# Optimization experiments

Hardware: AMD Instinct MI355X
Metric: run time of the kernel (lower is better)

Reference implementation:

```python
import jax, jax.numpy as jnp
import numpy as np

B, N, D, H = 2, 2048, 768, 12
HD = D // H  # 64


def apply_rotary_embed(x, thetas):
    # x: (..., N, HD), thetas: (N, HD) broadcast over leading dims
    x1, x2 = jnp.split(x, 2, axis=-1)
    x_rot = jnp.concatenate([-x2, x1], axis=-1)
    return x * jnp.cos(thetas) + x_rot * jnp.sin(thetas)


def setup_inputs() -> dict:
    key = jax.random.key(0)
    ks = jax.random.split(key, 5)
    s = 0.02
    return {
        "x": jax.random.normal(ks[0], (B, N, D), dtype=jnp.float32),
        "pos_embed": jax.random.normal(ks[1], (N, HD), dtype=jnp.float32),
        "Wqkv": jax.random.normal(ks[2], (3 * D, D), dtype=jnp.float32) * s,
        "Wproj": jax.random.normal(ks[3], (D, D), dtype=jnp.float32) * s,
        "bproj": jnp.zeros((D,), dtype=jnp.float32),
    }


def reference(x, pos_embed, Wqkv, Wproj, bproj):
    Bb, Nn, Dd = x.shape
    # fused QKV projection (torch Linear: x @ W.T), no bias
    qkv = jnp.einsum('bnd,ed->bne', x, Wqkv)                 # (B, N, 3D)
    qkv = qkv.reshape(Bb, Nn, 3, H, HD).transpose(2, 0, 3, 1, 4)  # (3, B, H, N, HD)
    q, k, v = qkv[0], qkv[1], qkv[2]
    # rotary embedding on q and k
    q = apply_rotary_embed(q, pos_embed)
    k = apply_rotary_embed(k, pos_embed)
    # scaled dot-product attention (non-causal, no mask, no dropout)
    scale = 1.0 / jnp.sqrt(jnp.asarray(HD, dtype=x.dtype))
    scores = jnp.einsum('bhqd,bhkd->bhqk', q, k) * scale     # (B, H, N, N)
    attn = jax.nn.softmax(scores, axis=-1)
    out = jnp.einsum('bhqk,bhkd->bhqd', attn, v)             # (B, H, N, HD)
    out = out.transpose(0, 2, 1, 3).reshape(Bb, Nn, Dd)      # (B, N, D)
    # output projection (with bias)
    return jnp.einsum('bnd,ed->bne', out, Wproj) + bproj
```

## Files before the change

### kernel.cpp

```cpp
#include <hip/hip_runtime.h>
#include <stdint.h>

typedef __attribute__((ext_vector_type(8))) short short8;
typedef __attribute__((ext_vector_type(4))) float floatx4;
typedef __attribute__((ext_vector_type(16))) float floatx16;

#define BB 2
#define NN 2048
#define DD 768
#define HH 12
#define HDD 64
#define MM (BB*NN)

__device__ __forceinline__ unsigned short f2bf(float f) {
  unsigned int u = __builtin_bit_cast(unsigned int, f);
  u += 0x7fffu + ((u >> 16) & 1u);
  return (unsigned short)(u >> 16);
}
__device__ __forceinline__ float bf2f(unsigned short u) {
  unsigned int v = ((unsigned int)u) << 16;
  return __builtin_bit_cast(float, v);
}

__device__ __forceinline__ void gld16(const unsigned short* g, unsigned short* l) {
  __builtin_amdgcn_global_load_lds(
      (const __attribute__((address_space(1))) void*)g,
      (__attribute__((address_space(3))) void*)l, 16, 0, 0);
}

__global__ void cvt_all(const float* __restrict__ x, const float* __restrict__ wq,
                        const float* __restrict__ wp, unsigned short* __restrict__ xb,
                        unsigned short* __restrict__ wqb, unsigned short* __restrict__ wpb) {
  const int n1 = MM*DD/4, n2 = 3*DD*DD/4, n3 = DD*DD/4;
  int i = blockIdx.x * blockDim.x + threadIdx.x;
  const float* s; unsigned short* d; int j;
  if (i < n1)            { s = x;  d = xb;  j = i; }
  else if (i < n1+n2)    { s = wq; d = wqb; j = i - n1; }
  else if (i < n1+n2+n3) { s = wp; d = wpb; j = i - n1 - n2; }
  else return;
  float4 v = reinterpret_cast<const float4*>(s)[j];
  unsigned int lo = (unsigned int)f2bf(v.x) | ((unsigned int)f2bf(v.y) << 16);
  unsigned int hi = (unsigned int)f2bf(v.z) | ((unsigned int)f2bf(v.w) << 16);
  reinterpret_cast<uint2*>(d)[j] = make_uint2(lo, hi);
}

template<int MODE, int MT>
__global__ __launch_bounds__(256) void gemm_bt(
    const unsigned short* __restrict__ A,
    const unsigned short* __restrict__ Bt,
    void* __restrict__ Cout, const float* __restrict__ bias,
    int Nn, int K,
    const float* __restrict__ pos,
    unsigned short* __restrict__ qb2, unsigned short* __restrict__ kb2,
    unsigned short* __restrict__ vb2)
{
  constexpr int MTC = MT / 32;
  __shared__ __align__(16) unsigned short as_[MT*32];
  __shared__ __align__(16) unsigned short bs_[128*32];
  const int t = threadIdx.x;
  const int w = t >> 6, lane = t & 63;
  const int quad = lane >> 4, l16 = lane & 15;
  const int wm = (w >> 1) * (MT/2), wn = (w & 1) * 64;
  const int m0 = blockIdx.y * MT, n0 = blockIdx.x * 128;

  const floatx4 fz = {0.f, 0.f, 0.f, 0.f};
  floatx4 acc[MTC][4];
#pragma unroll
  for (int mt = 0; mt < MTC; mt++)
#pragma unroll
    for (int nt = 0; nt < 4; nt++) acc[mt][nt] = fz;

  for (int k0 = 0; k0 < K; k0 += 32) {
    __syncthreads();
#pragma unroll
    for (int i = 0; i < MT/64; i++) {
      int c = t + i * 256;
      gld16(&A[(size_t)(m0 + (c >> 2))*K + k0 + (c & 3)*8], &as_[c*8]);
    }
#pragma unroll
    for (int i = 0; i < 2; i++) {
      int c = t + i * 256;
      gld16(&Bt[(size_t)(n0 + (c >> 2))*K + k0 + (c & 3)*8], &bs_[c*8]);
    }
    __syncthreads();
    short8 af[MTC], bfr[4];
#pragma unroll
    for (int mt = 0; mt < MTC; mt++)
      af[mt] = *reinterpret_cast<const short8*>(&as_[(wm + mt*16 + l16)*32 + quad*8]);
#pragma unroll
    for (int nt = 0; nt < 4; nt++)
      bfr[nt] = *reinterpret_cast<const short8*>(&bs_[(wn + nt*16 + l16)*32 + quad*8]);
#pragma unroll
    for (int mt = 0; mt < MTC; mt++)
#pragma unroll
      for (int nt = 0; nt < 4; nt++)
        acc[mt][nt] = __builtin_amdgcn_mfma_f32_16x16x32_bf16(af[mt], bfr[nt], acc[mt][nt], 0, 0, 0);
  }
  if (MODE == 2) {
    const int region = n0 / DD;
    const int nl0 = n0 - region * DD;
    const int head = (nl0 + wn) / HDD;
    if (region < 2) {
#pragma unroll
      for (int mt = 0; mt < MTC; mt++)
#pragma unroll
        for (int r = 0; r < 4; r++) {
          int gm = m0 + wm + mt*16 + quad*4 + r;
          int bq = gm >> 11, nseq = gm & (NN-1);
          size_t base = ((size_t)(bq*HH + head)*NN + nseq) * HDD;
#pragma unroll
          for (int nt = 0; nt < 2; nt++) {
            int hd = nt*16 + l16;
            float t1 = pos[nseq*HDD + hd], t2 = pos[nseq*HDD + hd + 32];
            float s1, c1, s2, c2;
            __sincosf(t1, &s1, &c1);
            __sincosf(t2, &s2, &c2);
            float a1 = acc[mt][nt][r], a2 = acc[mt][nt+2][r];
            if (region == 0) {
              qb2[base + hd]      = f2bf((a1*c1 - a2*s1) * 0.125f);
              qb2[base + hd + 32] = f2bf((a2*c2 + a1*s2) * 0.125f);
            } else {
              int sl1 = (hd >> 3) ^ (nseq & 7);
              int sl2 = ((hd >> 3) + 4) ^ (nseq & 7);
              kb2[base + sl1*8 + (hd & 7)] = f2bf(a1*c1 - a2*s1);
              kb2[base + sl2*8 + (hd & 7)] = f2bf(a2*c2 + a1*s2);
            }
          }
        }
    } else {
#pragma unroll
      for (int mt = 0; mt < MTC; mt++)
#pragma unroll
        for (int nt = 0; nt < 4; nt++) {
          int hd = nt*16 + l16;
          int seqb = m0 + wm + mt*16 + quad*4;
          int bq = seqb >> 11, nsb = seqb & (NN-1);
          unsigned int p0 = (unsigned int)f2bf(acc[mt][nt][0]) | ((unsigned int)f2bf(acc[mt][nt][1]) << 16);
          unsigned int p1 = (unsigned int)f2bf(acc[mt][nt][2]) | ((unsigned int)f2bf(acc[mt][nt][3]) << 16);
          int slot = ((nsb >> 3) & 15) ^ (hd & 7);
          size_t addr = ((size_t)(bq*HH + head)*HDD + hd) * NN + (nsb & ~127) + slot*8 + (nsb & 7);
          *(uint2*)&vb2[addr] = make_uint2(p0, p1);
        }
    }
  } else {
#pragma unroll
    for (int mt = 0; mt < MTC; mt++)
#pragma unroll
      for (int nt = 0; nt < 4; nt++)
#pragma unroll
        for (int r = 0; r < 4; r++) {
          int gm = m0 + wm + mt*16 + quad*4 + r;
          int gn = n0 + wn + nt*16 + l16;
          float v = acc[mt][nt][r];
          if (MODE == 0)
            reinterpret_cast<unsigned short*>(Cout)[(size_t)gm * Nn + gn] = f2bf(v);
          else
            reinterpret_cast<float*>(Cout)[(size_t)gm * Nn + gn] = v + bias[gn];
        }
  }
}

__global__ __launch_bounds__(256) void flash_attn(
    const unsigned short* __restrict__ qb, const unsigned short* __restrict__ kb,
    const unsigned short* __restrict__ vb, unsigned short* __restrict__ ob)
{
  __shared__ __align__(16) unsigned short ks[128*64];
  __shared__ __align__(16) unsigned short vt[64*128];
  __shared__ __align__(16) unsigned short ps[64*128];
  __shared__ __align__(16) float lsd[128];
  const int qt = blockIdx.x, bh = blockIdx.y;
  const int b = bh / HH, hh = bh % HH;
  const int t = threadIdx.x;
  const int w = t >> 6, lane = t & 63;
  const int l32 = lane & 31, hf = lane >> 5;
  const int gq = w >> 1;
  const int kh = w & 1;
  const int q0 = qt * 64;
  const size_t kbase = (size_t)bh * (NN*HDD);

  short8 qf[4];
  {
    const unsigned short* qp = &qb[((size_t)bh*NN + q0 + gq*32 + l32)*HDD + hf*8];
#pragma unroll
    for (int s = 0; s < 4; s++) qf[s] = *(const short8*)&qp[s*16];
  }
  floatx16 fz16;
#pragma unroll
  for (int z = 0; z < 16; z++) fz16[z] = 0.f;
  floatx16 oacc[2];
  oacc[0] = fz16; oacc[1] = fz16;
  float lrow = 0.f;

  for (int kt = 0; kt < NN/128; kt++) {
    __syncthreads();
#pragma unroll
    for (int i = 0; i < 4; i++) {
      int c = i*256 + t;
      gld16(&kb[kbase + (size_t)kt*8192 + c*8], &ks[c*8]);
      gld16(&vb[kbase + (size_t)(c >> 4)*NN + kt*128 + (c & 15)*8], &vt[c*8]);
    }
    __syncthreads();

    floatx16 sv[2];
#pragma unroll
    for (int tt = 0; tt < 2; tt++) {
      floatx16 acc;
#pragma unroll
      for (int z = 0; z < 16; z++) acc[z] = 0.f;
      int t2 = kh*2 + tt;
      int row = t2*32 + l32;
#pragma unroll
      for (int s = 0; s < 4; s++) {
        int cd = (2*s + hf) ^ (l32 & 7);
        short8 kf = *(const short8*)&ks[row*64 + cd*8];
        acc = __builtin_amdgcn_mfma_f32_32x32x16_bf16(kf, qf[s], acc, 0, 0, 0);
      }
      sv[tt] = acc;
    }
    float rs = 0.f;
    unsigned short* pr = &ps[(gq*32 + l32)*128];
#pragma unroll
    for (int tt = 0; tt < 2; tt++) {
      int t2 = kh*2 + tt;
      float pv_[16];
#pragma unroll
      for (int r = 0; r < 16; r++) { pv_[r] = __expf(sv[tt][r]); rs += pv_[r]; }
#pragma unroll
      for (int g = 0; g < 4; g++) {
        unsigned int x0 = __builtin_bit_cast(unsigned int, pv_[4*g+0]);
        unsigned int x1 = __builtin_bit_cast(unsigned int, pv_[4*g+1]);
        unsigned int x2 = __builtin_bit_cast(unsigned int, pv_[4*g+2]);
        unsigned int x3 = __builtin_bit_cast(unsigned int, pv_[4*g+3]);
        unsigned int lo = __builtin_amdgcn_perm(x1, x0, 0x07060302u);
        unsigned int hi = __builtin_amdgcn_perm(x3, x2, 0x07060302u);
        int slot = (t2*4 + g) ^ (l32 & 7);
        *(uint2*)&pr[slot*8 + hf*4] = make_uint2(lo, hi);
      }
    }
    rs += __shfl_xor(rs, 32);
    lrow += rs;
#pragma unroll
    for (int ss = 0; ss < 4; ss++) {
      int s2 = kh*4 + ss;
      int ca = (s2*2 + hf) ^ (l32 & 7);
      short8 pf = *(const short8*)&pr[ca*8];
#pragma unroll
      for (int ht = 0; ht < 2; ht++) {
        int hd = ht*32 + l32;
        short8 vf = *(const short8*)&vt[hd*128 + ca*8];
        oacc[ht] = __builtin_amdgcn_mfma_f32_32x32x16_bf16(pf, vf, oacc[ht], 0, 0, 0);
      }
    }
  }
  __syncthreads();
  float* om = (float*)ps;
  if (kh) {
    float* base = om + gq*2048;
#pragma unroll
    for (int ht = 0; ht < 2; ht++)
#pragma unroll
      for (int g = 0; g < 4; g++)
#pragma unroll
        for (int e = 0; e < 4; e++) {
          int ql = hf*4 + g*8 + e;
          base[ql*64 + ht*32 + l32] = oacc[ht][4*g+e];
        }
  }
  if (hf == 0) lsd[w*32 + l32] = lrow;
  __syncthreads();
  if (!kh) {
    float* base = om + gq*2048;
#pragma unroll
    for (int g = 0; g < 4; g++)
#pragma unroll
      for (int e = 0; e < 4; e++) {
        int ql = hf*4 + g*8 + e;
        float l = lsd[gq*64 + ql] + lsd[gq*64 + 32 + ql];
        float inv = 1.f / l;
        int qrow = q0 + gq*32 + ql;
#pragma unroll
        for (int ht = 0; ht < 2; ht++) {
          float v = oacc[ht][4*g+e] + base[ql*64 + ht*32 + l32];
          ob[((size_t)(b*NN + qrow))*DD + hh*HDD + ht*32 + l32] = f2bf(v * inv);
        }
      }
  }
}

extern "C" void kernel_launch(void* const* d_in, const int* in_sizes, int n_in,
                              void* d_out, int out_size, void* d_ws, size_t ws_size,
                              hipStream_t stream)
{
  const float* x     = (const float*)d_in[0];
  const float* pos   = (const float*)d_in[1];
  const float* Wqkv  = (const float*)d_in[2];
  const float* Wproj = (const float*)d_in[3];
  const float* bproj = (const float*)d_in[4];

  unsigned short* p = (unsigned short*)d_ws;
  unsigned short* xb     = p; p += (size_t)MM*DD;
  unsigned short* wqkvb  = p; p += (size_t)3*DD*DD;
  unsigned short* wprojb = p; p += (size_t)DD*DD;
  unsigned short* ob     = p; p += (size_t)MM*DD;
  unsigned short* qb     = p; p += (size_t)BB*HH*NN*HDD;
  unsigned short* kb     = p; p += (size_t)BB*HH*NN*HDD;
  unsigned short* vb     = p; p += (size_t)BB*HH*NN*HDD;

  const int ncvt = MM*DD/4 + 3*DD*DD/4 + DD*DD/4;
  cvt_all<<<ncvt/256, 256, 0, stream>>>(x, Wqkv, Wproj, xb, wqkvb, wprojb);

  gemm_bt<2,64><<<dim3(3*DD/128, MM/64), 256, 0, stream>>>(
      xb, wqkvb, nullptr, nullptr, 3*DD, DD, pos, qb, kb, vb);
  flash_attn<<<dim3(NN/64, BB*HH), 256, 0, stream>>>(qb, kb, vb, ob);
  gemm_bt<1,64><<<dim3(DD/128, MM/64), 256, 0, stream>>>(
      ob, wprojb, (float*)d_out, bproj, DD, DD, nullptr, nullptr, nullptr, nullptr);
}
```

Before: 172.4 us.

## Parameterize GEMM tiles, widen K-step to 64 with XOR-swizzled LDS

The GEMM kernel is templated on N-tile and K-step. The K-loop now stages 64-wide K slices, which halves the number of barrier pairs per K sweep, and LDS is XOR-swizzled per row to avoid bank conflicts on the short8 fragment reads. The output projection switches to 64-wide N tiles, doubling its grid to raise occupancy on the small GEMM. The cost is more LDS per block and extra index arithmetic for the swizzle.

```diff
diff --git a/kernel.cpp b/kernel.cpp
--- a/kernel.cpp
+++ b/kernel.cpp
@@ -44,7 +44,7 @@
   reinterpret_cast<uint2*>(d)[j] = make_uint2(lo, hi);
 }
 
-template<int MODE, int MT>
+template<int MODE, int MT, int NT, int BK>
 __global__ __launch_bounds__(256) void gemm_bt(
     const unsigned short* __restrict__ A,
     const unsigned short* __restrict__ Bt,
@@ -55,46 +55,61 @@
     unsigned short* __restrict__ vb2)
 {
   constexpr int MTC = MT / 32;
-  __shared__ __align__(16) unsigned short as_[MT*32];
-  __shared__ __align__(16) unsigned short bs_[128*32];
+  constexpr int NTC = NT / 32;
+  constexpr int PARTS = BK / 8;
+  __shared__ __align__(16) unsigned short as_[MT*BK];
+  __shared__ __align__(16) unsigned short bs_[NT*BK];
   const int t = threadIdx.x;
   const int w = t >> 6, lane = t & 63;
   const int quad = lane >> 4, l16 = lane & 15;
-  const int wm = (w >> 1) * (MT/2), wn = (w & 1) * 64;
-  const int m0 = blockIdx.y * MT, n0 = blockIdx.x * 128;
+  const int wm = (w >> 1) * (MT/2), wn = (w & 1) * (NT/2);
+  const int m0 = blockIdx.y * MT, n0 = blockIdx.x * NT;
 
   const floatx4 fz = {0.f, 0.f, 0.f, 0.f};
-  floatx4 acc[MTC][4];
+  floatx4 acc[MTC][NTC];
 #pragma unroll
   for (int mt = 0; mt < MTC; mt++)
 #pragma unroll
-    for (int nt = 0; nt < 4; nt++) acc[mt][nt] = fz;
-
-  for (int k0 = 0; k0 < K; k0 += 32) {
+    for (int nt = 0; nt < NTC; nt++) acc[mt][nt] = fz;
+
+  for (int k0 = 0; k0 < K; k0 += BK) {
     __syncthreads();
 #pragma unroll
-    for (int i = 0; i < MT/64; i++) {
+    for (int i = 0; i < MT*PARTS/256; i++) {
       int c = t + i * 256;
-      gld16(&A[(size_t)(m0 + (c >> 2))*K + k0 + (c & 3)*8], &as_[c*8]);
-    }
-#pragma unroll
-    for (int i = 0; i < 2; i++) {
+      int row = c / PARTS, part = c % PARTS;
+      int sp = part ^ (row & (PARTS-1));
+      gld16(&A[(size_t)(m0 + row)*K + k0 + sp*8], &as_[c*8]);
+    }
+#pragma unroll
+    for (int i = 0; i < NT*PARTS/256; i++) {
       int c = t + i * 256;
-      gld16(&Bt[(size_t)(n0 + (c >> 2))*K + k0 + (c & 3)*8], &bs_[c*8]);
+      int row = c / PARTS, part = c % PARTS;
+      int sp = part ^ (row & (PARTS-1));
+      gld16(&Bt[(size_t)(n0 + row)*K + k0 + sp*8], &bs_[c*8]);
     }
     __syncthreads();
-    short8 af[MTC], bfr[4];
-#pragma unroll
-    for (int mt = 0; mt < MTC; mt++)
-      af[mt] = *reinterpret_cast<const short8*>(&as_[(wm + mt*16 + l16)*32 + quad*8]);
-#pragma unroll
-    for (int nt = 0; nt < 4; nt++)
-      bfr[nt] = *reinterpret_cast<const short8*>(&bs_[(wn + nt*16 + l16)*32 + quad*8]);
-#pragma unroll
-    for (int mt = 0; mt < MTC; mt++)
-#pragma unroll
-      for (int nt = 0; nt < 4; nt++)
-        acc[mt][nt] = __builtin_amdgcn_mfma_f32_16x16x32_bf16(af[mt], bfr[nt], acc[mt][nt], 0, 0, 0);
+#pragma unroll
+    for (int kh = 0; kh < BK/32; kh++) {
+      short8 af[MTC], bfr[NTC];
+#pragma unroll
+      for (int mt = 0; mt < MTC; mt++) {
+        int row = wm + mt*16 + l16;
+        int slot = (kh*4 + quad) ^ (row & (PARTS-1));
+        af[mt] = *reinterpret_cast<const short8*>(&as_[row*BK + slot*8]);
+      }
+#pragma unroll
+      for (int nt = 0; nt < NTC; nt++) {
+        int row = wn + nt*16 + l16;
+        int slot = (kh*4 + quad) ^ (row & (PARTS-1));
+        bfr[nt] = *reinterpret_cast<const short8*>(&bs_[row*BK + slot*8]);
+      }
+#pragma unroll
+      for (int mt = 0; mt < MTC; mt++)
+#pragma unroll
+        for (int nt = 0; nt < NTC; nt++)
+          acc[mt][nt] = __builtin_amdgcn_mfma_f32_16x16x32_bf16(af[mt], bfr[nt], acc[mt][nt], 0, 0, 0);
+    }
   }
   if (MODE == 2) {
     const int region = n0 / DD;
@@ -131,7 +146,7 @@
 #pragma unroll
       for (int mt = 0; mt < MTC; mt++)
 #pragma unroll
-        for (int nt = 0; nt < 4; nt++) {
+        for (int nt = 0; nt < NTC; nt++) {
           int hd = nt*16 + l16;
           int seqb = m0 + wm + mt*16 + quad*4;
           int bq = seqb >> 11, nsb = seqb & (NN-1);
@@ -146,7 +161,7 @@
 #pragma unroll
     for (int mt = 0; mt < MTC; mt++)
 #pragma unroll
-      for (int nt = 0; nt < 4; nt++)
+      for (int nt = 0; nt < NTC; nt++)
 #pragma unroll
         for (int r = 0; r < 4; r++) {
           int gm = m0 + wm + mt*16 + quad*4 + r;
@@ -309,9 +324,9 @@
   const int ncvt = MM*DD/4 + 3*DD*DD/4 + DD*DD/4;
   cvt_all<<<ncvt/256, 256, 0, stream>>>(x, Wqkv, Wproj, xb, wqkvb, wprojb);
 
-  gemm_bt<2,64><<<dim3(3*DD/128, MM/64), 256, 0, stream>>>(
+  gemm_bt<2,64,128,64><<<dim3(3*DD/128, MM/64), 256, 0, stream>>>(
       xb, wqkvb, nullptr, nullptr, 3*DD, DD, pos, qb, kb, vb);
   flash_attn<<<dim3(NN/64, BB*HH), 256, 0, stream>>>(qb, kb, vb, ob);
-  gemm_bt<1,64><<<dim3(DD/128, MM/64), 256, 0, stream>>>(
+  gemm_bt<1,64,64,64><<<dim3(DD/64, MM/64), 256, 0, stream>>>(
       ob, wprojb, (float*)d_out, bproj, DD, DD, nullptr, nullptr, nullptr, nullptr);
 }
```

Result: faster. 160.7 us (-6.8%).
